# Kernel optimization log

Hardware: AMD Instinct MI355X
Metric: run time of the kernel (lower is better)

The kernel has to match this reference:

```python
import jax, jax.numpy as jnp
import numpy as np


def setup_inputs() -> dict:
    key = jax.random.key(0)
    k1, k2, k3, k4 = jax.random.split(key, 4)
    B, V, P, C, R, N, OUT = 8, 4096, 32, 32, 2, 16, 32  # N=(l_max+1)^2, l_max=3
    signal = jax.random.normal(k1, (B, V, C), dtype=jnp.float32)
    patches_idx = jax.random.randint(k2, (B, V, P), 0, V, dtype=jnp.int32)
    conv_kernel = jax.random.normal(k3, (B, V, P, R, N), dtype=jnp.float32)
    kernel_weights = jax.random.normal(k4, (OUT, C, R, N), dtype=jnp.float32) * 0.05
    biases = jnp.zeros((OUT,), dtype=jnp.float32)
    return {
        "signal": signal,
        "patches_idx": patches_idx,
        "conv_kernel": conv_kernel,
        "kernel_weights": kernel_weights,
        "biases": biases,
    }


def reference(signal, patches_idx, conv_kernel, kernel_weights, biases):
    # Gather per-vertex tree-neighbor patches (tf.gather_nd with batch idx):
    # signal [B,V,C], patches_idx [B,V,P] -> patches [B,V,P,C]
    patches = jax.vmap(lambda s, i: s[i])(signal, patches_idx)
    # Bilinear contraction with precomputed SH conv kernel: [B,V,P,R,N] x [B,V,P,C]
    y = jnp.einsum('bvprn,bvpc->bvcrn', conv_kernel, patches)
    # Learned weights contraction: [OUT,C,R,N] x [B,V,C,R,N] -> [B,V,OUT]
    y = jnp.einsum('ijrn,bvjrn->bvi', kernel_weights, y)
    y = y + biases
    return jax.nn.relu(y)
```

## Files before the change

### kernel.cpp

```cpp
#include <hip/hip_runtime.h>


typedef __attribute__((ext_vector_type(8))) short bf16x8;
typedef __attribute__((ext_vector_type(16))) float f32x16;
typedef __attribute__((ext_vector_type(4))) float f32x4;

__device__ __forceinline__ unsigned short f2bf_rne(float f) {
    union { float f; unsigned int u; } x;
    x.f = f;
    unsigned int u = x.u;
    return (unsigned short)((u + 0x7fffu + ((u >> 16) & 1u)) >> 16);
}
__device__ __forceinline__ unsigned short f2bf_rh(float f) {
    union { float f; unsigned int u; } x;
    x.f = f;
    return (unsigned short)((x.u + 0x8000u) >> 16);
}

__global__ __launch_bounds__(256) void prep_kernel(
        const float* __restrict__ W, const float* __restrict__ sig,
        unsigned short* __restrict__ Wf, unsigned short* __restrict__ sigbf) {
    int tid = blockIdx.x * 256 + threadIdx.x;
    if (tid < 32768) {
        int j = tid & 7;
        int l = (tid >> 3) & 63;
        int pair = tid >> 9;
        int s = pair >> 1;
        int t = pair & 1;
        int i = 16 * t + (l & 15);
        int crn = 32 * s + 8 * (l >> 4) + j;
        Wf[tid] = f2bf_rne(W[i * 1024 + crn]);
    } else {
        int e = (tid - 32768) * 8;
        if (e < 8 * 4096 * 32) {
            f32x4 a = *(const f32x4*)(sig + e);
            f32x4 b = *(const f32x4*)(sig + e + 4);
            bf16x8 v;
            v[0] = (short)f2bf_rne(a[0]); v[1] = (short)f2bf_rne(a[1]);
            v[2] = (short)f2bf_rne(a[2]); v[3] = (short)f2bf_rne(a[3]);
            v[4] = (short)f2bf_rne(b[0]); v[5] = (short)f2bf_rne(b[1]);
            v[6] = (short)f2bf_rne(b[2]); v[7] = (short)f2bf_rne(b[3]);
            *(bf16x8*)(sigbf + e) = v;
        }
    }
}

__global__ __launch_bounds__(256) void fused_kernel(
        const unsigned short* __restrict__ sigbf, const int* __restrict__ pidx,
        const float* __restrict__ ck, const unsigned short* __restrict__ Wf,
        const float* __restrict__ bias, float* __restrict__ out) {
    __shared__ __align__(16) unsigned short T_lds[16 * 1032];
    const int tid = threadIdx.x;
    const int l = tid & 63;
    const int w = tid >> 6;
    const int m0 = blockIdx.x * 16;
    const int b = m0 >> 12;
    const int cc = l & 31;
    const int g = l >> 5;
    const unsigned short* sgb = sigbf + (size_t)b * (4096 * 32);
    const unsigned short* ckh = (const unsigned short*)ck;

    for (int q = 0; q < 4; ++q) {
        const int bvl = w * 4 + q;
        const int m = m0 + bvl;
        const int* idxp = pidx + (size_t)m * 32;
        const size_t kbase = (size_t)m * 1024;
        f32x16 acc = {};
        #pragma unroll
        for (int half = 0; half < 2; ++half) {
            bf16x8 af, bfr;
            #pragma unroll
            for (int j = 0; j < 8; ++j) {
                const int p = half * 16 + 8 * g + j;
                const int row = idxp[p];
                af[j]  = (short)sgb[row * 32 + cc];
                bfr[j] = (short)ckh[((kbase + p * 32 + cc) << 1) | 1];
            }
            acc = __builtin_amdgcn_mfma_f32_32x32x16_bf16(af, bfr, acc, 0, 0, 0);
        }
        unsigned short* trow = T_lds + bvl * 1032 + cc + g * 4 * 32;
        #pragma unroll
        for (int r = 0; r < 16; ++r) {
            const int ct = (r & 3) + 8 * (r >> 2);
            trow[ct * 32] = f2bf_rh(acc[r]);
        }
    }
    __syncthreads();

    f32x4 acc0 = {}, acc1 = {};
    const int lg = l >> 4;
    const int ln = l & 15;
    #pragma unroll
    for (int si = 0; si < 8; ++si) {
        const int s = 8 * w + si;
        const bf16x8 af = *(const bf16x8*)(T_lds + ln * 1032 + s * 32 + 8 * lg);
        const bf16x8* wrow = (const bf16x8*)(Wf + (size_t)(s * 2) * 512);
        const bf16x8 b0 = wrow[l];
        const bf16x8 b1 = wrow[64 + l];
        acc0 = __builtin_amdgcn_mfma_f32_16x16x32_bf16(af, b0, acc0, 0, 0, 0);
        acc1 = __builtin_amdgcn_mfma_f32_16x16x32_bf16(af, b1, acc1, 0, 0, 0);
    }
    __syncthreads();

    float* red = (float*)T_lds;
    {
        f32x4* rp = (f32x4*)(red + w * 512);
        rp[l]      = acc0;
        rp[64 + l] = acc1;
    }
    __syncthreads();

    #pragma unroll
    for (int o0 = 0; o0 < 2; ++o0) {
        const int o = o0 * 256 + tid;
        float sum = red[o] + red[512 + o] + red[1024 + o] + red[1536 + o];
        const int t  = o >> 8;
        const int ll = (o >> 2) & 63;
        const int r  = o & 3;
        const int bv = ((ll >> 4) << 2) + r;
        const int i  = 16 * t + (ll & 15);
        sum += bias[i];
        out[(size_t)(m0 + bv) * 32 + i] = sum > 0.f ? sum : 0.f;
    }
}

extern "C" void kernel_launch(void* const* d_in, const int* in_sizes, int n_in,
                              void* d_out, int out_size, void* d_ws, size_t ws_size,
                              hipStream_t stream) {
    const float* sig  = (const float*)d_in[0];
    const int*   pidx = (const int*)d_in[1];
    const float* ck   = (const float*)d_in[2];
    const float* W    = (const float*)d_in[3];
    const float* bias = (const float*)d_in[4];
    float* out = (float*)d_out;
    unsigned short* Wf    = (unsigned short*)d_ws;
    unsigned short* sigbf = Wf + 32768;

    prep_kernel<<<640, 256, 0, stream>>>(W, sig, Wf, sigbf);
    fused_kernel<<<2048, 256, 0, stream>>>(sigbf, pidx, ck, Wf, bias, out);
}
```

Before: 40.35 us.

## Prefetch conv kernel and indices, stage through LDS, software-pipeline gathers

The conv_kernel rows are now loaded up front with coalesced 16-byte vector loads into registers, truncated to bf16 and staged per wave through padded LDS, replacing scattered 2-byte loads. Patch indices are copied into LDS once per block, and the signal gathers for the next vertex are issued before the MFMA work on the current one, so gather latency overlaps compute. This costs more registers (64 floats of kernel data per lane plus the gather buffers) and extra LDS, which may lower occupancy.

New measurement: 40.86 us. Within noise of the previous version (+1.3%).

```diff
diff --git a/kernel.cpp b/kernel.cpp
--- a/kernel.cpp
+++ b/kernel.cpp
@@ -2,8 +2,12 @@
 
 
 typedef __attribute__((ext_vector_type(8))) short bf16x8;
+typedef __attribute__((ext_vector_type(4))) short short4v;
 typedef __attribute__((ext_vector_type(16))) float f32x16;
 typedef __attribute__((ext_vector_type(4))) float f32x4;
+typedef __attribute__((ext_vector_type(4))) int int4v;
+
+#define KSTR 36
 
 __device__ __forceinline__ unsigned short f2bf_rne(float f) {
     union { float f; unsigned int u; } x;
@@ -50,6 +54,8 @@
         const float* __restrict__ ck, const unsigned short* __restrict__ Wf,
         const float* __restrict__ bias, float* __restrict__ out) {
     __shared__ __align__(16) unsigned short T_lds[16 * 1032];
+    __shared__ __align__(16) unsigned short K_lds[4 * 32 * KSTR];
+    __shared__ __align__(16) int idx_lds[512];
     const int tid = threadIdx.x;
     const int l = tid & 63;
     const int w = tid >> 6;
@@ -58,33 +64,71 @@
     const int cc = l & 31;
     const int g = l >> 5;
     const unsigned short* sgb = sigbf + (size_t)b * (4096 * 32);
-    const unsigned short* ckh = (const unsigned short*)ck;
+    unsigned short* kl = K_lds + w * 32 * KSTR;
 
+    f32x4 kreg[4][4];
+    #pragma unroll
     for (int q = 0; q < 4; ++q) {
-        const int bvl = w * 4 + q;
-        const int m = m0 + bvl;
-        const int* idxp = pidx + (size_t)m * 32;
-        const size_t kbase = (size_t)m * 1024;
+        const f32x4* kp = (const f32x4*)(ck + (size_t)(m0 + w * 4 + q) * 1024);
+        #pragma unroll
+        for (int t = 0; t < 4; ++t) kreg[q][t] = kp[t * 64 + l];
+    }
+    {
+        const int2* src = (const int2*)(pidx + (size_t)m0 * 32);
+        ((int2*)idx_lds)[tid] = src[tid];
+    }
+    __syncthreads();
+
+    auto issue_gathers = [&](int q, unsigned short (&gq)[16]) {
+        const int base = (w * 4 + q) * 32;
+        int4v ia = *(const int4v*)(idx_lds + base + 8 * g);
+        int4v ib = *(const int4v*)(idx_lds + base + 8 * g + 4);
+        int4v ic = *(const int4v*)(idx_lds + base + 16 + 8 * g);
+        int4v id = *(const int4v*)(idx_lds + base + 16 + 8 * g + 4);
+        #pragma unroll
+        for (int j = 0; j < 4; ++j) {
+            gq[j]      = sgb[ia[j] * 32 + cc];
+            gq[4 + j]  = sgb[ib[j] * 32 + cc];
+            gq[8 + j]  = sgb[ic[j] * 32 + cc];
+            gq[12 + j] = sgb[id[j] * 32 + cc];
+        }
+    };
+
+    auto compute_q = [&](int q, const unsigned short (&gq)[16], const f32x4 (&kq)[4]) {
+        #pragma unroll
+        for (int t = 0; t < 4; ++t) {
+            union { f32x4 f; unsigned int u[4]; } x;
+            x.f = kq[t];
+            short4v v = { (short)(x.u[0] >> 16), (short)(x.u[1] >> 16),
+                          (short)(x.u[2] >> 16), (short)(x.u[3] >> 16) };
+            *(short4v*)(kl + (t * 8 + (l >> 3)) * KSTR + 4 * (l & 7)) = v;
+        }
         f32x16 acc = {};
         #pragma unroll
         for (int half = 0; half < 2; ++half) {
             bf16x8 af, bfr;
             #pragma unroll
             for (int j = 0; j < 8; ++j) {
-                const int p = half * 16 + 8 * g + j;
-                const int row = idxp[p];
-                af[j]  = (short)sgb[row * 32 + cc];
-                bfr[j] = (short)ckh[((kbase + p * 32 + cc) << 1) | 1];
+                af[j]  = (short)gq[half * 8 + j];
+                bfr[j] = (short)kl[(half * 16 + 8 * g + j) * KSTR + cc];
             }
             acc = __builtin_amdgcn_mfma_f32_32x32x16_bf16(af, bfr, acc, 0, 0, 0);
         }
-        unsigned short* trow = T_lds + bvl * 1032 + cc + g * 4 * 32;
+        const int bvl = w * 4 + q;
+        unsigned short* trow = T_lds + bvl * 1032 + cc + g * 128;
         #pragma unroll
         for (int r = 0; r < 16; ++r) {
-            const int ct = (r & 3) + 8 * (r >> 2);
-            trow[ct * 32] = f2bf_rh(acc[r]);
+            trow[((r & 3) + 8 * (r >> 2)) * 32] = f2bf_rh(acc[r]);
         }
-    }
+    };
+
+    unsigned short g0[16], g1[16];
+    issue_gathers(0, g0);
+    issue_gathers(1, g1);
+    compute_q(0, g0, kreg[0]); issue_gathers(2, g0);
+    compute_q(1, g1, kreg[1]); issue_gathers(3, g1);
+    compute_q(2, g0, kreg[2]);
+    compute_q(3, g1, kreg[3]);
     __syncthreads();
 
     f32x4 acc0 = {}, acc1 = {};
```

## Use single-wave blocks of four rows and drop the cross-wave reduction

Applied to the files above, without the earlier changes.

Replaces 256-thread blocks of 16 rows, where the second GEMM is split along K across four waves and reduced through LDS, with 64-thread blocks of 4 rows. Each wave now does the whole K loop itself, which removes two barriers and the LDS reduction. The cost is that every block re-reads the full bf16 weight matrix, so L2 traffic for it rises about fourfold. The 16-row MFMA also carries only 4 useful rows, so second-stage matrix work rises about fourfold too. Smaller blocks should schedule more flexibly and overlap the memory-bound gather of the convolution kernel.

After: 49.11 us. 21.7% more time.

```diff
diff --git a/kernel.cpp b/kernel.cpp
--- a/kernel.cpp
+++ b/kernel.cpp
@@ -45,15 +45,13 @@
     }
 }
 
-__global__ __launch_bounds__(256) void fused_kernel(
+__global__ __launch_bounds__(64, 4) void fused_kernel(
         const unsigned short* __restrict__ sigbf, const int* __restrict__ pidx,
         const float* __restrict__ ck, const unsigned short* __restrict__ Wf,
         const float* __restrict__ bias, float* __restrict__ out) {
-    __shared__ __align__(16) unsigned short T_lds[16 * 1032];
-    const int tid = threadIdx.x;
-    const int l = tid & 63;
-    const int w = tid >> 6;
-    const int m0 = blockIdx.x * 16;
+    __shared__ __align__(16) unsigned short T_lds[4 * 1032];
+    const int l = threadIdx.x;
+    const int m0 = blockIdx.x * 4;
     const int b = m0 >> 12;
     const int cc = l & 31;
     const int g = l >> 5;
@@ -61,66 +59,49 @@
     const unsigned short* ckh = (const unsigned short*)ck;
 
     for (int q = 0; q < 4; ++q) {
-        const int bvl = w * 4 + q;
-        const int m = m0 + bvl;
+        const int m = m0 + q;
         const int* idxp = pidx + (size_t)m * 32;
-        const size_t kbase = (size_t)m * 1024;
+        const size_t kh = ((size_t)m * 1024) * 2 + 1;
         f32x16 acc = {};
         #pragma unroll
-        for (int half = 0; half < 2; ++half) {
+        for (int h = 0; h < 2; ++h) {
             bf16x8 af, bfr;
             #pragma unroll
             for (int j = 0; j < 8; ++j) {
-                const int p = half * 16 + 8 * g + j;
-                const int row = idxp[p];
-                af[j]  = (short)sgb[row * 32 + cc];
-                bfr[j] = (short)ckh[((kbase + p * 32 + cc) << 1) | 1];
+                const int p = h * 16 + 8 * g + j;
+                af[j]  = (short)sgb[idxp[p] * 32 + cc];
+                bfr[j] = (short)ckh[kh + (size_t)(p * 32 + cc) * 2];
             }
             acc = __builtin_amdgcn_mfma_f32_32x32x16_bf16(af, bfr, acc, 0, 0, 0);
         }
-        unsigned short* trow = T_lds + bvl * 1032 + cc + g * 4 * 32;
+        unsigned short* trow = T_lds + q * 1032 + cc + g * 128;
         #pragma unroll
-        for (int r = 0; r < 16; ++r) {
-            const int ct = (r & 3) + 8 * (r >> 2);
-            trow[ct * 32] = f2bf_rh(acc[r]);
-        }
+        for (int r = 0; r < 16; ++r)
+            trow[((r & 3) + 8 * (r >> 2)) * 32] = f2bf_rh(acc[r]);
     }
     __syncthreads();
 
     f32x4 acc0 = {}, acc1 = {};
-    const int lg = l >> 4;
-    const int ln = l & 15;
+    const int rowl = (l & 3) * 1032 + 8 * (l >> 4);
     #pragma unroll
-    for (int si = 0; si < 8; ++si) {
-        const int s = 8 * w + si;
-        const bf16x8 af = *(const bf16x8*)(T_lds + ln * 1032 + s * 32 + 8 * lg);
+    for (int s = 0; s < 32; ++s) {
+        const bf16x8 af = *(const bf16x8*)(T_lds + rowl + s * 32);
         const bf16x8* wrow = (const bf16x8*)(Wf + (size_t)(s * 2) * 512);
-        const bf16x8 b0 = wrow[l];
-        const bf16x8 b1 = wrow[64 + l];
-        acc0 = __builtin_amdgcn_mfma_f32_16x16x32_bf16(af, b0, acc0, 0, 0, 0);
-        acc1 = __builtin_amdgcn_mfma_f32_16x16x32_bf16(af, b1, acc1, 0, 0, 0);
+        acc0 = __builtin_amdgcn_mfma_f32_16x16x32_bf16(af, wrow[l],      acc0, 0, 0, 0);
+        acc1 = __builtin_amdgcn_mfma_f32_16x16x32_bf16(af, wrow[64 + l], acc1, 0, 0, 0);
     }
-    __syncthreads();
 
-    float* red = (float*)T_lds;
-    {
-        f32x4* rp = (f32x4*)(red + w * 512);
-        rp[l]      = acc0;
-        rp[64 + l] = acc1;
-    }
-    __syncthreads();
-
-    #pragma unroll
-    for (int o0 = 0; o0 < 2; ++o0) {
-        const int o = o0 * 256 + tid;
-        float sum = red[o] + red[512 + o] + red[1024 + o] + red[1536 + o];
-        const int t  = o >> 8;
-        const int ll = (o >> 2) & 63;
-        const int r  = o & 3;
-        const int bv = ((ll >> 4) << 2) + r;
-        const int i  = 16 * t + (ll & 15);
-        sum += bias[i];
-        out[(size_t)(m0 + bv) * 32 + i] = sum > 0.f ? sum : 0.f;
+    if (l < 16) {
+        const float b0 = bias[l];
+        const float b1 = bias[16 + l];
+        #pragma unroll
+        for (int r = 0; r < 4; ++r) {
+            float s0 = acc0[r] + b0;
+            float s1 = acc1[r] + b1;
+            float* orow = out + (size_t)(m0 + r) * 32;
+            orow[l]      = s0 > 0.f ? s0 : 0.f;
+            orow[16 + l] = s1 > 0.f ? s1 : 0.f;
+        }
     }
 }
 
@@ -137,5 +118,5 @@
     unsigned short* sigbf = Wf + 32768;
 
     prep_kernel<<<640, 256, 0, stream>>>(W, sig, Wf, sigbf);
-    fused_kernel<<<2048, 256, 0, stream>>>(sigbf, pidx, ck, Wf, bias, out);
+    fused_kernel<<<8192, 64, 0, stream>>>(sigbf, pidx, ck, Wf, bias, out);
 }
```

## Stage conv kernel through LDS with coalesced loads and halve vertices per block

Applied to the files above, without the earlier changes.

Each block now handles 8 vertices instead of 16, with twice as many blocks. The conv kernel tile is read with coalesced 16-byte loads, truncated to bf16 high halves, and staged in LDS, where the old code read each bf16 half with a scattered 2-byte load. Patch indices are loaded up front and all gathered signal values are issued before the barrier to raise memory-level parallelism. This uses more registers (the rows and ga arrays); launch_bounds asks for 4 blocks per SM to cap that. In the second GEMM, the 16 MFMA rows are filled with the 8 vertices duplicated, so half of that matrix work is wasted.

New measurement: 38.84 us. 3.7% less time.

```diff
diff --git a/kernel.cpp b/kernel.cpp
--- a/kernel.cpp
+++ b/kernel.cpp
@@ -2,6 +2,7 @@
 
 
 typedef __attribute__((ext_vector_type(8))) short bf16x8;
+typedef __attribute__((ext_vector_type(4))) short short4v;
 typedef __attribute__((ext_vector_type(16))) float f32x16;
 typedef __attribute__((ext_vector_type(4))) float f32x4;
 
@@ -45,45 +46,76 @@
     }
 }
 
-__global__ __launch_bounds__(256) void fused_kernel(
+__global__ __launch_bounds__(256, 4) void fused_kernel(
         const unsigned short* __restrict__ sigbf, const int* __restrict__ pidx,
         const float* __restrict__ ck, const unsigned short* __restrict__ Wf,
         const float* __restrict__ bias, float* __restrict__ out) {
-    __shared__ __align__(16) unsigned short T_lds[16 * 1032];
+    __shared__ __align__(16) unsigned short ckb[8 * 1024];
+    __shared__ __align__(16) unsigned short T_lds[8 * 1032];
     const int tid = threadIdx.x;
     const int l = tid & 63;
-    const int w = tid >> 6;
-    const int m0 = blockIdx.x * 16;
+    const int g = l >> 5;
+    const int cc = l & 31;
+    const int wu = __builtin_amdgcn_readfirstlane(tid >> 6);
+    const int m0 = blockIdx.x * 8;
     const int b = m0 >> 12;
-    const int cc = l & 31;
-    const int g = l >> 5;
     const unsigned short* sgb = sigbf + (size_t)b * (4096 * 32);
-    const unsigned short* ckh = (const unsigned short*)ck;
 
-    for (int q = 0; q < 4; ++q) {
-        const int bvl = w * 4 + q;
-        const int m = m0 + bvl;
-        const int* idxp = pidx + (size_t)m * 32;
-        const size_t kbase = (size_t)m * 1024;
+    f32x4 st[8];
+    {
+        const f32x4* ckv = (const f32x4*)(ck + (size_t)m0 * 1024);
+        #pragma unroll
+        for (int i = 0; i < 8; ++i) st[i] = ckv[i * 256 + tid];
+    }
+    int rows[64];
+    {
+        const int* idxp = pidx + (size_t)(m0 + 2 * wu) * 32;
+        #pragma unroll
+        for (int k = 0; k < 64; ++k) rows[k] = idxp[k];
+    }
+    unsigned short ga[32];
+    #pragma unroll
+    for (int q = 0; q < 2; ++q) {
+        #pragma unroll
+        for (int h = 0; h < 2; ++h) {
+            #pragma unroll
+            for (int j = 0; j < 8; ++j) {
+                const int rlo = rows[q * 32 + h * 16 + j];
+                const int rhi = rows[q * 32 + h * 16 + 8 + j];
+                const int row = g ? rhi : rlo;
+                ga[q * 16 + h * 8 + j] = sgb[row * 32 + cc];
+            }
+        }
+    }
+    #pragma unroll
+    for (int i = 0; i < 8; ++i) {
+        union { f32x4 f; unsigned int u[4]; } x;
+        x.f = st[i];
+        short4v v = { (short)(x.u[0] >> 16), (short)(x.u[1] >> 16),
+                      (short)(x.u[2] >> 16), (short)(x.u[3] >> 16) };
+        *(short4v*)(ckb + (i * 256 + tid) * 4) = v;
+    }
+    __syncthreads();
+
+    #pragma unroll
+    for (int q = 0; q < 2; ++q) {
+        const unsigned short* ct = ckb + (2 * wu + q) * 1024;
         f32x16 acc = {};
         #pragma unroll
-        for (int half = 0; half < 2; ++half) {
+        for (int h = 0; h < 2; ++h) {
             bf16x8 af, bfr;
             #pragma unroll
             for (int j = 0; j < 8; ++j) {
-                const int p = half * 16 + 8 * g + j;
-                const int row = idxp[p];
-                af[j]  = (short)sgb[row * 32 + cc];
-                bfr[j] = (short)ckh[((kbase + p * 32 + cc) << 1) | 1];
+                const int p = h * 16 + 8 * g + j;
+                af[j]  = (short)ga[q * 16 + h * 8 + j];
+                bfr[j] = (short)ct[p * 32 + cc];
             }
             acc = __builtin_amdgcn_mfma_f32_32x32x16_bf16(af, bfr, acc, 0, 0, 0);
         }
-        unsigned short* trow = T_lds + bvl * 1032 + cc + g * 4 * 32;
+        unsigned short* trow = T_lds + (2 * wu + q) * 1032 + cc + g * 128;
         #pragma unroll
-        for (int r = 0; r < 16; ++r) {
-            const int ct = (r & 3) + 8 * (r >> 2);
-            trow[ct * 32] = f2bf_rh(acc[r]);
-        }
+        for (int r = 0; r < 16; ++r)
+            trow[((r & 3) + 8 * (r >> 2)) * 32] = f2bf_rh(acc[r]);
     }
     __syncthreads();
 
@@ -92,8 +124,8 @@
     const int ln = l & 15;
     #pragma unroll
     for (int si = 0; si < 8; ++si) {
-        const int s = 8 * w + si;
-        const bf16x8 af = *(const bf16x8*)(T_lds + ln * 1032 + s * 32 + 8 * lg);
+        const int s = 8 * wu + si;
+        const bf16x8 af = *(const bf16x8*)(T_lds + (ln & 7) * 1032 + s * 32 + 8 * lg);
         const bf16x8* wrow = (const bf16x8*)(Wf + (size_t)(s * 2) * 512);
         const bf16x8 b0 = wrow[l];
         const bf16x8 b1 = wrow[64 + l];
@@ -104,21 +136,22 @@
 
     float* red = (float*)T_lds;
     {
-        f32x4* rp = (f32x4*)(red + w * 512);
+        f32x4* rp = (f32x4*)(red + wu * 512);
         rp[l]      = acc0;
         rp[64 + l] = acc1;
     }
     __syncthreads();
 
-    #pragma unroll
-    for (int o0 = 0; o0 < 2; ++o0) {
-        const int o = o0 * 256 + tid;
+    {
+        const int bv  = tid >> 5;
+        const int i   = tid & 31;
+        const int t   = i >> 4;
+        const int col = i & 15;
+        const int lgi = bv >> 2;
+        const int r   = bv & 3;
+        const int li  = lgi * 16 + col;
+        const int o   = t * 256 + li * 4 + r;
         float sum = red[o] + red[512 + o] + red[1024 + o] + red[1536 + o];
-        const int t  = o >> 8;
-        const int ll = (o >> 2) & 63;
-        const int r  = o & 3;
-        const int bv = ((ll >> 4) << 2) + r;
-        const int i  = 16 * t + (ll & 15);
         sum += bias[i];
         out[(size_t)(m0 + bv) * 32 + i] = sum > 0.f ? sum : 0.f;
     }
@@ -137,5 +170,5 @@
     unsigned short* sigbf = Wf + 32768;
 
     prep_kernel<<<640, 256, 0, stream>>>(W, sig, Wf, sigbf);
-    fused_kernel<<<2048, 256, 0, stream>>>(sigbf, pidx, ck, Wf, bias, out);
+    fused_kernel<<<4096, 256, 0, stream>>>(sigbf, pidx, ck, Wf, bias, out);
 }
```
